# Kernel optimization log

Measured on AMD Instinct MI355X. Metric: run time of the kernel, lower is better.

The kernel has to match this reference:

```python
import jax, jax.numpy as jnp
import numpy as np

NEG_INF = -1e30


def setup_inputs() -> dict:
    key = jax.random.key(0)
    kq, kk, kv, ks = jax.random.split(key, 4)
    B, H, S, D = 2, 16, 2048, 64
    return {
        "q": jax.random.normal(kq, (B, H, S, D), dtype=jnp.float32),
        "k": jax.random.normal(kk, (B, H, S, D), dtype=jnp.float32),
        "v": jax.random.normal(kv, (B, H, S, D), dtype=jnp.float32),
        "sink_weights": jax.random.normal(ks, (H,), dtype=jnp.float32),
        "sliding_window": 1024,
    }


def reference(q, k, v, sink_weights, sliding_window):
    """Sliding-window causal attention with a learnable attention-sink logit.

    Equivalent to FlexAttention.forward with sink_weights given: an extra kv
    position (the sink) is appended whose score is replaced by sink_weights[h]
    and whose value is zero -> it only adds mass to the softmax denominator.
    """
    B, H, S_q, D = q.shape
    S_kv = k.shape[2]
    scale = 1.0 / np.sqrt(D)

    # [B, H, S_q, S_kv] raw scores
    scores = jnp.einsum("bhqd,bhkd->bhqk", q, k) * scale

    q_idx = jnp.arange(S_q)[:, None]
    kv_idx = jnp.arange(S_kv)[None, :]
    keep = (kv_idx <= q_idx) & (q_idx - kv_idx <= sliding_window)  # [S_q, S_kv]
    scores = jnp.where(keep[None, None], scores, NEG_INF)

    # sink column: per-head learnable logit, always visible
    sink_col = jnp.broadcast_to(
        sink_weights[None, :, None, None], (B, H, S_q, 1)
    )
    logits = jnp.concatenate([scores, sink_col], axis=-1)  # [B,H,S_q,S_kv+1]

    probs = jax.nn.softmax(logits, axis=-1)
    # sink value is zero, so only the first S_kv prob columns hit v
    out = jnp.einsum("bhqk,bhkd->bhqd", probs[..., :S_kv], v)
    return out
```

## Files before the change

### kernel.cpp

```cpp
#include <hip/hip_runtime.h>
#include <cstdint>


typedef __bf16 bf16x8 __attribute__((ext_vector_type(8)));
typedef __bf16 bf16x4 __attribute__((ext_vector_type(4)));
typedef float  f32x16 __attribute__((ext_vector_type(16)));

#define NT 256
#define NEG_BIG (-3.0e38f)

typedef const __attribute__((address_space(1))) void gvoid;
typedef __attribute__((address_space(3))) void lvoid;

__device__ __forceinline__ void glds16(const void* g, void* l) {
    __builtin_amdgcn_global_load_lds((gvoid*)g, (lvoid*)l, 16, 0, 0);
}

__device__ __forceinline__ int swz(int row, int gran) {
    return row * 64 + ((gran ^ ((row >> 1) & 7)) << 3);
}

__device__ __forceinline__ bf16x4 xswap32(bf16x4 v) {
    union { bf16x4 v; int i[2]; } u;
    u.v = v;
    u.i[0] = __shfl_xor(u.i[0], 32, 64);
    u.i[1] = __shfl_xor(u.i[1], 32, 64);
    return u.v;
}

__device__ const int SEG_N[32] = {
  2,1,1,2,2,1,2,1, 2,1,2,1,1,2,1,1, 1,1,2,1,1,2,1,1, 1,1,2,1,1,2,1,1};
__device__ const int SEG_IT[32][2] = {
  {0,1},{2,0},{3,0},{3,4},{4,5},{5,0},{5,6},{6,0},
  {6,7},{7,0},{7,8},{8,0},{8,0},{8,9},{9,0},{9,0},
  {10,0},{10,0},{10,11},{11,0},{11,0},{11,12},{12,0},{12,0},
  {13,0},{13,0},{13,14},{14,0},{14,0},{14,15},{15,0},{15,0}};
__device__ const int SEG_J0[32][2] = {
  {0,0},{0,0},{0,0},{7,0},{6,0},{3,0},{10,0},{5,0},
  {12,0},{5,0},{12,0},{2,0},{9,0},{16,0},{5,0},{12,0},
  {0,0},{7,0},{14,0},{3,0},{10,0},{17,0},{6,0},{12,0},
  {0,0},{7,0},{14,0},{3,0},{10,0},{17,0},{6,0},{12,0}};
__device__ const int SEG_J1[32][2] = {
  {2,4},{6,0},{7,0},{8,6},{10,3},{10,0},{12,5},{12,0},
  {14,5},{12,0},{16,2},{9,0},{16,0},{18,5},{12,0},{18,0},
  {7,0},{14,0},{18,3},{10,0},{17,0},{18,6},{12,0},{18,0},
  {7,0},{14,0},{18,3},{10,0},{17,0},{18,6},{12,0},{18,0}};
__device__ const int SEG_SX[32][2] = {
  {0,0},{0,0},{0,0},{1,0},{1,0},{1,0},{2,0},{1,0},
  {2,0},{1,0},{2,0},{1,0},{2,0},{3,0},{1,0},{2,0},
  {0,0},{1,0},{2,0},{1,0},{2,0},{3,0},{1,0},{2,0},
  {0,0},{1,0},{2,0},{1,0},{2,0},{3,0},{1,0},{2,0}};
__device__ const int NSEG16[16]      = {1,1,1,2,2,3,3,3,4,3,3,4,3,3,4,3};
__device__ const int SLOT_BASE16[16] = {0,1,2,3,5,7,10,13,16,20,23,26,30,33,36,40};
#define NSLOT 43

__global__ __launch_bounds__(256) void flex_r11_prep(
    const float* __restrict__ K, const float* __restrict__ V,
    float* __restrict__ IMG, const int H, const int S)
{
    const int t  = threadIdx.x;
    const int bh = blockIdx.x >> 5;
    const int kt = blockIdx.x & 31;
    const size_t basebh = (size_t)bh * S * 64;
    const float4* kp4 = (const float4*)(K + basebh);
    const float4* vp4 = (const float4*)(V + basebh);
    __bf16* img = (__bf16*)IMG + ((size_t)bh * 32 + kt) * 8192;

    #pragma unroll
    for (int i = 0; i < 4; ++i) {
        const int flat = i * 256 + t;
        const int key = flat >> 4, dd = flat & 15;
        float4 f = kp4[kt * 1024 + flat];
        bf16x4 b = { (__bf16)f.x, (__bf16)f.y, (__bf16)f.z, (__bf16)f.w };
        *(bf16x4*)&img[swz(key, dd >> 1) + (dd & 1) * 4] = b;
    }
    const int dgi = t & 15, kgi = t >> 4;
    float4 a0 = vp4[kt * 1024 + (4 * kgi + 0) * 16 + dgi];
    float4 a1 = vp4[kt * 1024 + (4 * kgi + 1) * 16 + dgi];
    float4 a2 = vp4[kt * 1024 + (4 * kgi + 2) * 16 + dgi];
    float4 a3 = vp4[kt * 1024 + (4 * kgi + 3) * 16 + dgi];
    bf16x4 w0 = { (__bf16)a0.x, (__bf16)a1.x, (__bf16)a2.x, (__bf16)a3.x };
    bf16x4 w1 = { (__bf16)a0.y, (__bf16)a1.y, (__bf16)a2.y, (__bf16)a3.y };
    bf16x4 w2 = { (__bf16)a0.z, (__bf16)a1.z, (__bf16)a2.z, (__bf16)a3.z };
    bf16x4 w3 = { (__bf16)a0.w, (__bf16)a1.w, (__bf16)a2.w, (__bf16)a3.w };
    const int gv = kgi >> 1, ov = (kgi & 1) * 4;
    __bf16* imgV = img + 4096;
    *(bf16x4*)&imgV[swz(4 * dgi + 0, gv) + ov] = w0;
    *(bf16x4*)&imgV[swz(4 * dgi + 1, gv) + ov] = w1;
    *(bf16x4*)&imgV[swz(4 * dgi + 2, gv) + ov] = w2;
    *(bf16x4*)&imgV[swz(4 * dgi + 3, gv) + ov] = w3;
}

__global__ __launch_bounds__(NT, 4) void flex_r11_main(
    const float* __restrict__ Q, const float* __restrict__ SINKW,
    const int* __restrict__ SWIN, void* __restrict__ WS,
    const float* __restrict__ IMG, const int H, const int S)
{
    const int t    = threadIdx.x;
    const int lane = t & 63;
    const int w    = t >> 6;
    const int c    = lane & 31;
    const int hl   = lane >> 5;
    const int W    = SWIN[0];
    const float scale = 0.125f;

    const int NBH = gridDim.x / 32;
    const int bh  = blockIdx.x / 32;
    const int bin = blockIdx.x - bh * 32;
    const int h   = bh % H;
    const float sw = SINKW[h];

    __shared__ __align__(16) __bf16 k_lds[2][64 * 64];
    __shared__ __align__(16) __bf16 v_lds[2][64 * 64];

    const size_t basebh = (size_t)bh * S * 64;
    const __bf16* kvimg = (const __bf16*)IMG + (size_t)bh * 32 * 8192;
    __bf16* O_ws  = (__bf16*)WS;
    float2* ml_ws = (float2*)((char*)WS + (size_t)NBH * NSLOT * 16384);

    const int wb = (t >> 6) << 10;
    const int ns = SEG_N[bin];

    {
        const int it0  = SEG_IT[bin][0];
        const int ktA0 = (2 * it0 - 16 > 0) ? (2 * it0 - 16) : 0;
        const int kt   = ktA0 + SEG_J0[bin][0];
        const char* g  = (const char*)(kvimg + (size_t)kt * 8192);
        char* lk = (char*)&k_lds[0][0];
        char* lv = (char*)&v_lds[0][0];
        glds16(g +         t * 16, lk + wb);
        glds16(g +  4096 + t * 16, lk + wb + 4096);
        glds16(g +  8192 + t * 16, lv + wb);
        glds16(g + 12288 + t * 16, lv + wb + 4096);
    }

    int par = 0;

    for (int s = 0; s < ns; ++s) {
        const int item = SEG_IT[bin][s];
        const int j0   = SEG_J0[bin][s];
        const int j1   = SEG_J1[bin][s];
        const int sidx = SEG_SX[bin][s];
        const int ktA  = (2 * item - 16 > 0) ? (2 * item - 16) : 0;
        const int qw0  = item * 128 + 32 * w;
        const int qi   = qw0 + c;

        bf16x8 bq[4];
        {
            const float4* qp4 = (const float4*)(Q + basebh + (size_t)qi * 64);
            #pragma unroll
            for (int ks = 0; ks < 4; ++ks) {
                float4 f0 = qp4[4 * ks + 2 * hl];
                float4 f1 = qp4[4 * ks + 2 * hl + 1];
                bq[ks][0] = (__bf16)(f0.x * scale); bq[ks][1] = (__bf16)(f0.y * scale);
                bq[ks][2] = (__bf16)(f0.z * scale); bq[ks][3] = (__bf16)(f0.w * scale);
                bq[ks][4] = (__bf16)(f1.x * scale); bq[ks][5] = (__bf16)(f1.y * scale);
                bq[ks][6] = (__bf16)(f1.z * scale); bq[ks][7] = (__bf16)(f1.w * scale);
            }
        }

        float mrun = (sidx == 0) ? sw : NEG_BIG;
        float lrun = (sidx == 0) ? 1.0f : 0.0f;
        f32x16 accO0, accO1;
        #pragma unroll
        for (int i = 0; i < 16; ++i) { accO0[i] = 0.0f; accO1[i] = 0.0f; }

        for (int j = j0; j < j1; ++j) {
            const int k0 = (ktA + j) * 64;

            __syncthreads();

            int nkt = -1;
            if (j + 1 < j1) nkt = ktA + j + 1;
            else if (s + 1 < ns) {
                const int it2  = SEG_IT[bin][s + 1];
                const int ktA2 = (2 * it2 - 16 > 0) ? (2 * it2 - 16) : 0;
                nkt = ktA2 + SEG_J0[bin][s + 1];
            }
            if (nkt >= 0) {
                const int np = par ^ 1;
                const char* g = (const char*)(kvimg + (size_t)nkt * 8192);
                char* lk = (char*)&k_lds[np][0];
                char* lv = (char*)&v_lds[np][0];
                glds16(g +         t * 16, lk + wb);
                glds16(g +  4096 + t * 16, lk + wb + 4096);
                glds16(g +  8192 + t * 16, lv + wb);
                glds16(g + 12288 + t * 16, lv + wb + 4096);
            }

            const __bf16* kb = k_lds[par];
            const __bf16* vb = v_lds[par];
            f32x16 accS0, accS1;
            #pragma unroll
            for (int i = 0; i < 16; ++i) { accS0[i] = 0.0f; accS1[i] = 0.0f; }
            #pragma unroll
            for (int ks = 0; ks < 4; ++ks) {
                bf16x8 ka0 = *(const bf16x8*)&kb[swz(c,      2 * ks + hl)];
                bf16x8 ka1 = *(const bf16x8*)&kb[swz(32 + c, 2 * ks + hl)];
                accS0 = __builtin_amdgcn_mfma_f32_32x32x16_bf16(ka0, bq[ks], accS0, 0, 0, 0);
                accS1 = __builtin_amdgcn_mfma_f32_32x32x16_bf16(ka1, bq[ks], accS1, 0, 0, 0);
            }

            const bool interior = (k0 + 63 <= qw0) && (qw0 + 31 - k0 <= W);
            if (!interior) {
                #pragma unroll
                for (int rg = 0; rg < 16; ++rg) {
                    const int kb2 = (rg & 3) + 8 * (rg >> 2) + 4 * hl;
                    const int ki0 = k0 + kb2, ki1 = k0 + 32 + kb2;
                    if (!((ki0 <= qi) && (qi - ki0 <= W))) accS0[rg] = -1e30f;
                    if (!((ki1 <= qi) && (qi - ki1 <= W))) accS1[rg] = -1e30f;
                }
            }

            float mx = accS0[0];
            #pragma unroll
            for (int i = 1; i < 16; ++i) mx = fmaxf(mx, accS0[i]);
            #pragma unroll
            for (int i = 0; i < 16; ++i) mx = fmaxf(mx, accS1[i]);
            mx = fmaxf(mx, __shfl_xor(mx, 32, 64));
            const float mnew  = fmaxf(mrun, mx);
            const float alpha = __expf(mrun - mnew);
            float ps = 0.0f;
            #pragma unroll
            for (int i = 0; i < 16; ++i) { float p = __expf(accS0[i] - mnew); accS0[i] = p; ps += p; }
            #pragma unroll
            for (int i = 0; i < 16; ++i) { float p = __expf(accS1[i] - mnew); accS1[i] = p; ps += p; }
            ps += __shfl_xor(ps, 32, 64);
            lrun = lrun * alpha + ps;
            mrun = mnew;
            #pragma unroll
            for (int i = 0; i < 16; ++i) { accO0[i] *= alpha; accO1[i] *= alpha; }

            bf16x4 qA = { (__bf16)accS0[0],  (__bf16)accS0[1],  (__bf16)accS0[2],  (__bf16)accS0[3]  };
            bf16x4 qB = { (__bf16)accS0[4],  (__bf16)accS0[5],  (__bf16)accS0[6],  (__bf16)accS0[7]  };
            bf16x4 qC = { (__bf16)accS0[8],  (__bf16)accS0[9],  (__bf16)accS0[10], (__bf16)accS0[11] };
            bf16x4 qD = { (__bf16)accS0[12], (__bf16)accS0[13], (__bf16)accS0[14], (__bf16)accS0[15] };
            bf16x4 qE = { (__bf16)accS1[0],  (__bf16)accS1[1],  (__bf16)accS1[2],  (__bf16)accS1[3]  };
            bf16x4 qF = { (__bf16)accS1[4],  (__bf16)accS1[5],  (__bf16)accS1[6],  (__bf16)accS1[7]  };
            bf16x4 qG = { (__bf16)accS1[8],  (__bf16)accS1[9],  (__bf16)accS1[10], (__bf16)accS1[11] };
            bf16x4 qH = { (__bf16)accS1[12], (__bf16)accS1[13], (__bf16)accS1[14], (__bf16)accS1[15] };
            bf16x4 r0 = xswap32(hl ? qA : qB);
            bf16x4 r1 = xswap32(hl ? qC : qD);
            bf16x4 r2 = xswap32(hl ? qE : qF);
            bf16x4 r3 = xswap32(hl ? qG : qH);
            bf16x4 lo0 = hl ? r0 : qA, hi0 = hl ? qB : r0;
            bf16x4 lo1 = hl ? r1 : qC, hi1 = hl ? qD : r1;
            bf16x4 lo2 = hl ? r2 : qE, hi2 = hl ? qF : r2;
            bf16x4 lo3 = hl ? r3 : qG, hi3 = hl ? qH : r3;
            bf16x8 bp[4];
            #pragma unroll
            for (int e = 0; e < 4; ++e) {
                bp[0][e] = lo0[e]; bp[0][4+e] = hi0[e];
                bp[1][e] = lo1[e]; bp[1][4+e] = hi1[e];
                bp[2][e] = lo2[e]; bp[2][4+e] = hi2[e];
                bp[3][e] = lo3[e]; bp[3][4+e] = hi3[e];
            }

            #pragma unroll
            for (int ks = 0; ks < 4; ++ks) {
                bf16x8 va0 = *(const bf16x8*)&vb[swz(c,      2 * ks + hl)];
                bf16x8 va1 = *(const bf16x8*)&vb[swz(32 + c, 2 * ks + hl)];
                accO0 = __builtin_amdgcn_mfma_f32_32x32x16_bf16(va0, bp[ks], accO0, 0, 0, 0);
                accO1 = __builtin_amdgcn_mfma_f32_32x32x16_bf16(va1, bp[ks], accO1, 0, 0, 0);
            }

            par ^= 1;
        }

        const int slot = bh * NSLOT + SLOT_BASE16[item] + sidx;
        const int qrel = 32 * w + c;
        if (hl == 0) ml_ws[(size_t)slot * 128 + qrel] = make_float2(mrun, lrun);
        __bf16* Os = O_ws + (size_t)slot * 8192 + (size_t)qrel * 64;
        #pragma unroll
        for (int qd = 0; qd < 4; ++qd) {
            const int d0 = 8 * qd + 4 * hl;
            bf16x4 b0 = { (__bf16)accO0[4*qd+0], (__bf16)accO0[4*qd+1],
                          (__bf16)accO0[4*qd+2], (__bf16)accO0[4*qd+3] };
            bf16x4 b1 = { (__bf16)accO1[4*qd+0], (__bf16)accO1[4*qd+1],
                          (__bf16)accO1[4*qd+2], (__bf16)accO1[4*qd+3] };
            *(bf16x4*)&Os[d0]      = b0;
            *(bf16x4*)&Os[32 + d0] = b1;
        }
    }
}

__global__ __launch_bounds__(256) void flex_r11_combine(
    const void* __restrict__ WS, float* __restrict__ OUT, const int H, const int S)
{
    const int NBH  = gridDim.x / 16;
    const int bi   = blockIdx.x;
    const int bh   = bi >> 4;
    const int item = bi & 15;
    const int ns   = NSEG16[item];
    const int t    = threadIdx.x;
    const int q    = t >> 1;
    const int half = t & 1;

    const __bf16* O_ws  = (const __bf16*)WS;
    const float2* ml_ws = (const float2*)((const char*)WS + (size_t)NBH * NSLOT * 16384);
    const int base = bh * NSLOT + SLOT_BASE16[item];

    float m[4], lv[4], a[4];
    float mst = NEG_BIG;
    for (int s = 0; s < ns; ++s) {
        float2 e = ml_ws[(size_t)(base + s) * 128 + q];
        m[s] = e.x; lv[s] = e.y;
        mst = fmaxf(mst, m[s]);
    }
    float lst = 0.0f;
    for (int s = 0; s < ns; ++s) { a[s] = __expf(m[s] - mst); lst += a[s] * lv[s]; }
    const float inv = 1.0f / lst;

    float acc[32];
    #pragma unroll
    for (int i = 0; i < 32; ++i) acc[i] = 0.0f;
    for (int s = 0; s < ns; ++s) {
        const __bf16* Os = O_ws + (size_t)(base + s) * 8192 + (size_t)q * 64 + 32 * half;
        const float as = a[s];
        #pragma unroll
        for (int v8 = 0; v8 < 4; ++v8) {
            bf16x8 o = *(const bf16x8*)&Os[8 * v8];
            #pragma unroll
            for (int jj = 0; jj < 8; ++jj) acc[8 * v8 + jj] += as * (float)o[jj];
        }
    }

    float* dst = OUT + (size_t)bh * S * 64 + (size_t)(item * 128 + q) * 64 + 32 * half;
    #pragma unroll
    for (int v4 = 0; v4 < 8; ++v4) {
        float4 f = { acc[4*v4+0] * inv, acc[4*v4+1] * inv,
                     acc[4*v4+2] * inv, acc[4*v4+3] * inv };
        *(float4*)&dst[4 * v4] = f;
    }
}

extern "C" void kernel_launch(void* const* d_in, const int* in_sizes, int n_in,
                              void* d_out, int out_size, void* d_ws, size_t ws_size,
                              hipStream_t stream) {
    const float* q     = (const float*)d_in[0];
    const float* k     = (const float*)d_in[1];
    const float* v     = (const float*)d_in[2];
    const float* sinkw = (const float*)d_in[3];
    const int*   swin  = (const int*)d_in[4];
    float* out = (float*)d_out;

    const int H = in_sizes[3];
    const int S = 2048;
    const int B = in_sizes[0] / (H * S * 64);
    const int NBH = B * H;

    flex_r11_prep<<<dim3(NBH * 32), 256, 0, stream>>>(k, v, out, H, S);
    flex_r11_main<<<dim3(NBH * 32), NT, 0, stream>>>(q, sinkw, swin, d_ws, out, H, S);
    flex_r11_combine<<<dim3(NBH * 16), 256, 0, stream>>>(d_ws, out, H, S);
}
```

Before: 145.2 us.

## Load K/V fragments directly from global into registers, drop LDS staging

The main kernel no longer stages K/V tiles through double-buffered LDS with barriers. Each wave now loads its MFMA fragments straight from a row-major bf16 image in global memory into registers, prefetching the next K tile during the PV step. The change also remaps blocks across XCDs so that blocks sharing a batch-head land on the same L2, skips the online-softmax rescale unless the max grows past a threshold, raises MFMA priority with setprio, and lowers occupancy to 3 blocks. The cost is redundant global/L2 traffic, since each wave reads the same K/V tile, and higher register pressure.

```diff
diff --git a/kernel.cpp b/kernel.cpp
--- a/kernel.cpp
+++ b/kernel.cpp
@@ -8,17 +8,6 @@
 
 #define NT 256
 #define NEG_BIG (-3.0e38f)
-
-typedef const __attribute__((address_space(1))) void gvoid;
-typedef __attribute__((address_space(3))) void lvoid;
-
-__device__ __forceinline__ void glds16(const void* g, void* l) {
-    __builtin_amdgcn_global_load_lds((gvoid*)g, (lvoid*)l, 16, 0, 0);
-}
-
-__device__ __forceinline__ int swz(int row, int gran) {
-    return row * 64 + ((gran ^ ((row >> 1) & 7)) << 3);
-}
 
 __device__ __forceinline__ bf16x4 xswap32(bf16x4 v) {
     union { bf16x4 v; int i[2]; } u;
@@ -54,7 +43,7 @@
 __device__ const int SLOT_BASE16[16] = {0,1,2,3,5,7,10,13,16,20,23,26,30,33,36,40};
 #define NSLOT 43
 
-__global__ __launch_bounds__(256) void flex_r11_prep(
+__global__ __launch_bounds__(256) void flex_r12_prep(
     const float* __restrict__ K, const float* __restrict__ V,
     float* __restrict__ IMG, const int H, const int S)
 {
@@ -69,12 +58,11 @@
     #pragma unroll
     for (int i = 0; i < 4; ++i) {
         const int flat = i * 256 + t;
-        const int key = flat >> 4, dd = flat & 15;
         float4 f = kp4[kt * 1024 + flat];
         bf16x4 b = { (__bf16)f.x, (__bf16)f.y, (__bf16)f.z, (__bf16)f.w };
-        *(bf16x4*)&img[swz(key, dd >> 1) + (dd & 1) * 4] = b;
-    }
-    const int dgi = t & 15, kgi = t >> 4;
+        *(bf16x4*)&img[4 * flat] = b;
+    }
+    const int kgi = t & 15, dgi = t >> 4;
     float4 a0 = vp4[kt * 1024 + (4 * kgi + 0) * 16 + dgi];
     float4 a1 = vp4[kt * 1024 + (4 * kgi + 1) * 16 + dgi];
     float4 a2 = vp4[kt * 1024 + (4 * kgi + 2) * 16 + dgi];
@@ -83,15 +71,14 @@
     bf16x4 w1 = { (__bf16)a0.y, (__bf16)a1.y, (__bf16)a2.y, (__bf16)a3.y };
     bf16x4 w2 = { (__bf16)a0.z, (__bf16)a1.z, (__bf16)a2.z, (__bf16)a3.z };
     bf16x4 w3 = { (__bf16)a0.w, (__bf16)a1.w, (__bf16)a2.w, (__bf16)a3.w };
-    const int gv = kgi >> 1, ov = (kgi & 1) * 4;
     __bf16* imgV = img + 4096;
-    *(bf16x4*)&imgV[swz(4 * dgi + 0, gv) + ov] = w0;
-    *(bf16x4*)&imgV[swz(4 * dgi + 1, gv) + ov] = w1;
-    *(bf16x4*)&imgV[swz(4 * dgi + 2, gv) + ov] = w2;
-    *(bf16x4*)&imgV[swz(4 * dgi + 3, gv) + ov] = w3;
-}
-
-__global__ __launch_bounds__(NT, 4) void flex_r11_main(
+    *(bf16x4*)&imgV[(4 * dgi + 0) * 64 + 4 * kgi] = w0;
+    *(bf16x4*)&imgV[(4 * dgi + 1) * 64 + 4 * kgi] = w1;
+    *(bf16x4*)&imgV[(4 * dgi + 2) * 64 + 4 * kgi] = w2;
+    *(bf16x4*)&imgV[(4 * dgi + 3) * 64 + 4 * kgi] = w3;
+}
+
+__global__ __launch_bounds__(NT, 3) void flex_r12_main(
     const float* __restrict__ Q, const float* __restrict__ SINKW,
     const int* __restrict__ SWIN, void* __restrict__ WS,
     const float* __restrict__ IMG, const int H, const int S)
@@ -104,37 +91,42 @@
     const int W    = SWIN[0];
     const float scale = 0.125f;
 
-    const int NBH = gridDim.x / 32;
-    const int bh  = blockIdx.x / 32;
-    const int bin = blockIdx.x - bh * 32;
-    const int h   = bh % H;
+    const int NBH = gridDim.x >> 5;
+    int bh, bin;
+    if ((NBH & 7) == 0) {
+        const int G    = NBH >> 3;
+        const int xcd  = blockIdx.x & 7;
+        const int rest = blockIdx.x >> 3;
+        const int g    = rest % G;
+        bin = rest / G;
+        bh  = (g << 3) + xcd;
+    } else {
+        bh  = blockIdx.x >> 5;
+        bin = blockIdx.x & 31;
+    }
+    const int h  = bh % H;
     const float sw = SINKW[h];
-
-    __shared__ __align__(16) __bf16 k_lds[2][64 * 64];
-    __shared__ __align__(16) __bf16 v_lds[2][64 * 64];
 
     const size_t basebh = (size_t)bh * S * 64;
     const __bf16* kvimg = (const __bf16*)IMG + (size_t)bh * 32 * 8192;
     __bf16* O_ws  = (__bf16*)WS;
     float2* ml_ws = (float2*)((char*)WS + (size_t)NBH * NSLOT * 16384);
 
-    const int wb = (t >> 6) << 10;
+    const int rofs = c * 64 + hl * 8;
     const int ns = SEG_N[bin];
 
+    bf16x8 kf[8];
     {
         const int it0  = SEG_IT[bin][0];
         const int ktA0 = (2 * it0 - 16 > 0) ? (2 * it0 - 16) : 0;
-        const int kt   = ktA0 + SEG_J0[bin][0];
-        const char* g  = (const char*)(kvimg + (size_t)kt * 8192);
-        char* lk = (char*)&k_lds[0][0];
-        char* lv = (char*)&v_lds[0][0];
-        glds16(g +         t * 16, lk + wb);
-        glds16(g +  4096 + t * 16, lk + wb + 4096);
-        glds16(g +  8192 + t * 16, lv + wb);
-        glds16(g + 12288 + t * 16, lv + wb + 4096);
-    }
-
-    int par = 0;
+        const int kt0  = ktA0 + SEG_J0[bin][0];
+        const __bf16* kr = kvimg + (size_t)kt0 * 8192 + rofs;
+        #pragma unroll
+        for (int ks = 0; ks < 4; ++ks) {
+            kf[2*ks]   = *(const bf16x8*)(kr + ks * 16);
+            kf[2*ks+1] = *(const bf16x8*)(kr + 2048 + ks * 16);
+        }
+    }
 
     for (int s = 0; s < ns; ++s) {
         const int item = SEG_IT[bin][s];
@@ -167,39 +159,28 @@
 
         for (int j = j0; j < j1; ++j) {
             const int k0 = (ktA + j) * 64;
-
-            __syncthreads();
-
-            int nkt = -1;
-            if (j + 1 < j1) nkt = ktA + j + 1;
-            else if (s + 1 < ns) {
-                const int it2  = SEG_IT[bin][s + 1];
-                const int ktA2 = (2 * it2 - 16 > 0) ? (2 * it2 - 16) : 0;
-                nkt = ktA2 + SEG_J0[bin][s + 1];
-            }
-            if (nkt >= 0) {
-                const int np = par ^ 1;
-                const char* g = (const char*)(kvimg + (size_t)nkt * 8192);
-                char* lk = (char*)&k_lds[np][0];
-                char* lv = (char*)&v_lds[np][0];
-                glds16(g +         t * 16, lk + wb);
-                glds16(g +  4096 + t * 16, lk + wb + 4096);
-                glds16(g +  8192 + t * 16, lv + wb);
-                glds16(g + 12288 + t * 16, lv + wb + 4096);
-            }
-
-            const __bf16* kb = k_lds[par];
-            const __bf16* vb = v_lds[par];
+            const __bf16* tb = kvimg + (size_t)(ktA + j) * 8192;
+
+            bf16x8 vf[8];
+            {
+                const __bf16* vr = tb + 4096 + rofs;
+                #pragma unroll
+                for (int ks = 0; ks < 4; ++ks) {
+                    vf[2*ks]   = *(const bf16x8*)(vr + ks * 16);
+                    vf[2*ks+1] = *(const bf16x8*)(vr + 2048 + ks * 16);
+                }
+            }
+
             f32x16 accS0, accS1;
             #pragma unroll
             for (int i = 0; i < 16; ++i) { accS0[i] = 0.0f; accS1[i] = 0.0f; }
+            __builtin_amdgcn_s_setprio(1);
             #pragma unroll
             for (int ks = 0; ks < 4; ++ks) {
-                bf16x8 ka0 = *(const bf16x8*)&kb[swz(c,      2 * ks + hl)];
-                bf16x8 ka1 = *(const bf16x8*)&kb[swz(32 + c, 2 * ks + hl)];
-                accS0 = __builtin_amdgcn_mfma_f32_32x32x16_bf16(ka0, bq[ks], accS0, 0, 0, 0);
-                accS1 = __builtin_amdgcn_mfma_f32_32x32x16_bf16(ka1, bq[ks], accS1, 0, 0, 0);
-            }
+                accS0 = __builtin_amdgcn_mfma_f32_32x32x16_bf16(kf[2*ks],   bq[ks], accS0, 0, 0, 0);
+                accS1 = __builtin_amdgcn_mfma_f32_32x32x16_bf16(kf[2*ks+1], bq[ks], accS1, 0, 0, 0);
+            }
+            __builtin_amdgcn_s_setprio(0);
 
             const bool interior = (k0 + 63 <= qw0) && (qw0 + 31 - k0 <= W);
             if (!interior) {
@@ -212,24 +193,32 @@
                 }
             }
 
-            float mx = accS0[0];
-            #pragma unroll
-            for (int i = 1; i < 16; ++i) mx = fmaxf(mx, accS0[i]);
-            #pragma unroll
-            for (int i = 0; i < 16; ++i) mx = fmaxf(mx, accS1[i]);
+            float q4[8];
+            #pragma unroll
+            for (int i = 0; i < 4; ++i) {
+                q4[i]   = fmaxf(fmaxf(accS0[4*i], accS0[4*i+1]),
+                                fmaxf(accS0[4*i+2], accS0[4*i+3]));
+                q4[4+i] = fmaxf(fmaxf(accS1[4*i], accS1[4*i+1]),
+                                fmaxf(accS1[4*i+2], accS1[4*i+3]));
+            }
+            float mx = fmaxf(fmaxf(fmaxf(q4[0], q4[1]), fmaxf(q4[2], q4[3])),
+                             fmaxf(fmaxf(q4[4], q4[5]), fmaxf(q4[6], q4[7])));
             mx = fmaxf(mx, __shfl_xor(mx, 32, 64));
-            const float mnew  = fmaxf(mrun, mx);
-            const float alpha = __expf(mrun - mnew);
+            if (!__all(mx <= mrun + 8.0f)) {
+                const float mnew  = fmaxf(mrun, mx);
+                const float alpha = __expf(mrun - mnew);
+                lrun *= alpha;
+                #pragma unroll
+                for (int i = 0; i < 16; ++i) { accO0[i] *= alpha; accO1[i] *= alpha; }
+                mrun = mnew;
+            }
             float ps = 0.0f;
             #pragma unroll
-            for (int i = 0; i < 16; ++i) { float p = __expf(accS0[i] - mnew); accS0[i] = p; ps += p; }
-            #pragma unroll
-            for (int i = 0; i < 16; ++i) { float p = __expf(accS1[i] - mnew); accS1[i] = p; ps += p; }
+            for (int i = 0; i < 16; ++i) { float p = __expf(accS0[i] - mrun); accS0[i] = p; ps += p; }
+            #pragma unroll
+            for (int i = 0; i < 16; ++i) { float p = __expf(accS1[i] - mrun); accS1[i] = p; ps += p; }
             ps += __shfl_xor(ps, 32, 64);
-            lrun = lrun * alpha + ps;
-            mrun = mnew;
-            #pragma unroll
-            for (int i = 0; i < 16; ++i) { accO0[i] *= alpha; accO1[i] *= alpha; }
+            lrun += ps;
 
             bf16x4 qA = { (__bf16)accS0[0],  (__bf16)accS0[1],  (__bf16)accS0[2],  (__bf16)accS0[3]  };
             bf16x4 qB = { (__bf16)accS0[4],  (__bf16)accS0[5],  (__bf16)accS0[6],  (__bf16)accS0[7]  };
@@ -256,15 +245,29 @@
                 bp[3][e] = lo3[e]; bp[3][4+e] = hi3[e];
             }
 
+            int nkt = -1;
+            if (j + 1 < j1) nkt = ktA + j + 1;
+            else if (s + 1 < ns) {
+                const int it2  = SEG_IT[bin][s + 1];
+                const int ktA2 = (2 * it2 - 16 > 0) ? (2 * it2 - 16) : 0;
+                nkt = ktA2 + SEG_J0[bin][s + 1];
+            }
+            if (nkt >= 0) {
+                const __bf16* krn = kvimg + (size_t)nkt * 8192 + rofs;
+                #pragma unroll
+                for (int ks = 0; ks < 4; ++ks) {
+                    kf[2*ks]   = *(const bf16x8*)(krn + ks * 16);
+                    kf[2*ks+1] = *(const bf16x8*)(krn + 2048 + ks * 16);
+                }
+            }
+
+            __builtin_amdgcn_s_setprio(1);
             #pragma unroll
             for (int ks = 0; ks < 4; ++ks) {
-                bf16x8 va0 = *(const bf16x8*)&vb[swz(c,      2 * ks + hl)];
-                bf16x8 va1 = *(const bf16x8*)&vb[swz(32 + c, 2 * ks + hl)];
-                accO0 = __builtin_amdgcn_mfma_f32_32x32x16_bf16(va0, bp[ks], accO0, 0, 0, 0);
-                accO1 = __builtin_amdgcn_mfma_f32_32x32x16_bf16(va1, bp[ks], accO1, 0, 0, 0);
-            }
-
-            par ^= 1;
+                accO0 = __builtin_amdgcn_mfma_f32_32x32x16_bf16(vf[2*ks],   bp[ks], accO0, 0, 0, 0);
+                accO1 = __builtin_amdgcn_mfma_f32_32x32x16_bf16(vf[2*ks+1], bp[ks], accO1, 0, 0, 0);
+            }
+            __builtin_amdgcn_s_setprio(0);
         }
 
         const int slot = bh * NSLOT + SLOT_BASE16[item] + sidx;
@@ -284,7 +287,7 @@
     }
 }
 
-__global__ __launch_bounds__(256) void flex_r11_combine(
+__global__ __launch_bounds__(256) void flex_r12_combine(
     const void* __restrict__ WS, float* __restrict__ OUT, const int H, const int S)
 {
     const int NBH  = gridDim.x / 16;
@@ -349,7 +352,7 @@
     const int B = in_sizes[0] / (H * S * 64);
     const int NBH = B * H;
 
-    flex_r11_prep<<<dim3(NBH * 32), 256, 0, stream>>>(k, v, out, H, S);
-    flex_r11_main<<<dim3(NBH * 32), NT, 0, stream>>>(q, sinkw, swin, d_ws, out, H, S);
-    flex_r11_combine<<<dim3(NBH * 16), 256, 0, stream>>>(d_ws, out, H, S);
-}
+    flex_r12_prep<<<dim3(NBH * 32), 256, 0, stream>>>(k, v, out, H, S);
+    flex_r12_main<<<dim3(NBH * 32), NT, 0, stream>>>(q, sinkw, swin, d_ws, out, H, S);
+    flex_r12_combine<<<dim3(NBH * 16), 256, 0, stream>>>(d_ws, out, H, S);
+}
```

Result: slower. 188.2 us (+29.7%).
